# Kernel tuning notes

Hardware: AMD Instinct MI355X
Metric: run time of the kernel (lower is better)

## Reference

```python
import jax, jax.numpy as jnp
import numpy as np

B, F, D = 32, 4096, 256
ALPHA = 0.001


def setup_inputs() -> dict:
    key = jax.random.key(0)
    ks = jax.random.split(key, 9)
    s = 1.0 / np.sqrt(D)
    return {
        "q": jax.random.normal(ks[0], (B, F, D), dtype=jnp.float32),
        "k": jax.random.normal(ks[1], (B, F, D), dtype=jnp.float32),
        "v": jax.random.normal(ks[2], (B, F, D), dtype=jnp.float32),
        "Wq": jax.random.normal(ks[3], (D, D), dtype=jnp.float32) * s,
        "bq": jax.random.normal(ks[4], (D,), dtype=jnp.float32) * 0.01,
        "Wk": jax.random.normal(ks[5], (D, D), dtype=jnp.float32) * s,
        "bk": jax.random.normal(ks[6], (D,), dtype=jnp.float32) * 0.01,
        "Wv": jax.random.normal(ks[7], (D, D), dtype=jnp.float32) * s,
        "bv": jax.random.normal(ks[8], (D,), dtype=jnp.float32) * 0.01,
    }


def reference(q, k, v, Wq, bq, Wk, bk, Wv, bv):
    # nn.Linear: x @ W.T + b
    queries = q @ Wq.T + bq            # [b, f, d]
    keys = k @ Wk.T + bk               # [b, f, d]
    values = v @ Wv.T + bv             # [b, f, d]
    # batched Gram matrix + ridge term
    key_sym = jnp.einsum("bfd,bfe->bde", keys, keys)          # [b, d, d]
    key_sym = key_sym + ALPHA * jnp.eye(D, dtype=key_sym.dtype)
    key_sym_inv = jnp.linalg.inv(key_sym)                      # [b, d, d]
    kkik = jnp.einsum("bde,bfe->bdf", key_sym_inv, keys)       # [b, d, f]
    kkikv = jnp.einsum("bdf,bfe->bde", kkik, values)           # [b, d, d]
    itn = jax.nn.softmax(kkikv, axis=2)                        # sigma=True; softmax over dim 2
    h = jnp.einsum("bfd,bde->be", queries, itn)                # [b, d]
    return h
```

## Files before the change

kernel.cpp:

```cpp
#include <hip/hip_runtime.h>
#include <math.h>

#define FDIM 4096
#define DDIM 256
#define ALPHA_R 0.001f
#define SVH (3 * 32 * 256)

typedef __attribute__((ext_vector_type(8))) short short8;
typedef __attribute__((ext_vector_type(4))) float f32x4;

__device__ __forceinline__ unsigned cvt_pk_bf16(float lo_e, float hi_e) {
  unsigned r;
  asm("v_cvt_pk_bf16_f32 %0, %1, %2" : "=v"(r) : "v"(lo_e), "v"(hi_e));
  return r;
}

__device__ __forceinline__ void hilo8(const float* x, uint4& H, uint4& L) {
  unsigned h0 = cvt_pk_bf16(x[0], x[1]);
  unsigned h1 = cvt_pk_bf16(x[2], x[3]);
  unsigned h2 = cvt_pk_bf16(x[4], x[5]);
  unsigned h3 = cvt_pk_bf16(x[6], x[7]);
  unsigned l0 = cvt_pk_bf16(x[0] - __uint_as_float(h0 << 16),
                            x[1] - __uint_as_float(h0 & 0xFFFF0000u));
  unsigned l1 = cvt_pk_bf16(x[2] - __uint_as_float(h1 << 16),
                            x[3] - __uint_as_float(h1 & 0xFFFF0000u));
  unsigned l2 = cvt_pk_bf16(x[4] - __uint_as_float(h2 << 16),
                            x[5] - __uint_as_float(h2 & 0xFFFF0000u));
  unsigned l3 = cvt_pk_bf16(x[6] - __uint_as_float(h3 << 16),
                            x[7] - __uint_as_float(h3 & 0xFFFF0000u));
  H = make_uint4(h0, h1, h2, h3);
  L = make_uint4(l0, l1, l2, l3);
}

__global__ __launch_bounds__(256) void gram_fused(const float* __restrict__ kg,
                                                  const float* __restrict__ vg,
                                                  const float* __restrict__ qg,
                                                  float* __restrict__ Gp0,
                                                  float* __restrict__ Gp1,
                                                  float* __restrict__ svec,
                                                  float* __restrict__ part) {
  int flat = blockIdx.x;
  int tid = threadIdx.x;

  if (flat >= 1024) {
    int cs = flat - 1024;
    int chunk = cs & 15, b = cs >> 4;
    int rg = tid >> 6, dq = tid & 63;
    const float* p = qg + ((size_t)b * FDIM + chunk * 256 + rg) * DDIM + dq * 4;
    float4 s = make_float4(0.f, 0.f, 0.f, 0.f);
    for (int i = 0; i < 64; ++i) {
      float4 t = *(const float4*)(p + (size_t)i * 4 * DDIM);
      s.x += t.x; s.y += t.y; s.z += t.z; s.w += t.w;
    }
    __shared__ __align__(16) float redq[4][64][4];
    *(float4*)&redq[rg][dq][0] = s;
    __syncthreads();
    if (rg == 0) {
      float4 a0 = *(float4*)&redq[0][dq][0];
      float4 a1 = *(float4*)&redq[1][dq][0];
      float4 a2 = *(float4*)&redq[2][dq][0];
      float4 a3 = *(float4*)&redq[3][dq][0];
      float4 t = make_float4(a0.x + a1.x + a2.x + a3.x, a0.y + a1.y + a2.y + a3.y,
                             a0.z + a1.z + a2.z + a3.z, a0.w + a1.w + a2.w + a3.w);
      *(float4*)(part + ((size_t)chunk * 32 + b) * DDIM + dq * 4) = t;
    }
    return;
  }

  int xcd = flat & 7, s = flat >> 3;
  int b = xcd * 4 + (s >> 5);
  int rem = s & 31;
  int tile = rem >> 1;
  int half = rem & 1;
  int tm = tile >> 2, tn = tile & 3;
  int mBase = tm * 64, nBase = tn * 64;
  const float* Kb = kg + (size_t)b * FDIM * DDIM;
  const float* Vb = vg + (size_t)b * FDIM * DDIM;

  __shared__ __align__(16) unsigned short Ah[64][40], Al[64][40];
  __shared__ __align__(16) unsigned short Bh[64][40], Bl[64][40];
  __shared__ __align__(16) unsigned short Ch[64][40], Cl[64][40];
  __shared__ float sred[4][68];

  int w = tid >> 6, lane = tid & 63;
  int wr = w >> 1, wc = w & 1;
  int lrow = lane & 15;
  int kof = (lane >> 4) * 8;

  const float* pA = Kb + mBase + lane;
  const float* pB = Kb + nBase + lane;
  const float* pC = Vb + nBase + lane;

  bool doK = (tn == 0), doV = (tm == 0);
  float sK = 0.f, sV = 0.f;
  int fBase = half * 2048;

  float xa[8], xb[8], xc[8];
  auto loadIter = [&](int it) {
    int f = fBase + it * 32 + w * 8;
#pragma unroll
    for (int j = 0; j < 8; ++j) {
      xa[j] = pA[(size_t)(f + j) * DDIM];
      xb[j] = pB[(size_t)(f + j) * DDIM];
      xc[j] = pC[(size_t)(f + j) * DDIM];
    }
  };
  auto stash = [&](const float* x, unsigned short (*H)[40], unsigned short (*L)[40]) {
    uint4 hh, ll;
    hilo8(x, hh, ll);
    *(uint4*)&H[lane][w * 8] = hh;
    *(uint4*)&L[lane][w * 8] = ll;
  };

  f32x4 acc0[2][2], acc1[2][2];
#pragma unroll
  for (int mt = 0; mt < 2; ++mt)
#pragma unroll
    for (int nt = 0; nt < 2; ++nt) {
      acc0[mt][nt] = (f32x4){0.f, 0.f, 0.f, 0.f};
      acc1[mt][nt] = (f32x4){0.f, 0.f, 0.f, 0.f};
    }

  loadIter(0);
  for (int it = 0; it < 64; ++it) {
    __syncthreads();
    stash(xa, Ah, Al);
    stash(xb, Bh, Bl);
    stash(xc, Ch, Cl);
    if (doK) sK += ((xa[0] + xa[1]) + (xa[2] + xa[3])) + ((xa[4] + xa[5]) + (xa[6] + xa[7]));
    if (doV) sV += ((xc[0] + xc[1]) + (xc[2] + xc[3])) + ((xc[4] + xc[5]) + (xc[6] + xc[7]));
    __syncthreads();
    if (it < 63) loadIter(it + 1);

    short8 bh[2], bl[2], ch[2], cl[2];
#pragma unroll
    for (int nt = 0; nt < 2; ++nt) {
      int rB = wc * 32 + nt * 16 + lrow;
      bh[nt] = *(const short8*)&Bh[rB][kof];
      bl[nt] = *(const short8*)&Bl[rB][kof];
      ch[nt] = *(const short8*)&Ch[rB][kof];
      cl[nt] = *(const short8*)&Cl[rB][kof];
    }
    __builtin_amdgcn_s_setprio(1);
#pragma unroll
    for (int mt = 0; mt < 2; ++mt) {
      int rA = wr * 32 + mt * 16 + lrow;
      short8 ah = *(const short8*)&Ah[rA][kof];
      short8 al = *(const short8*)&Al[rA][kof];
#pragma unroll
      for (int nt = 0; nt < 2; ++nt) {
        f32x4 t = acc0[mt][nt];
        t = __builtin_amdgcn_mfma_f32_16x16x32_bf16(ah, bh[nt], t, 0, 0, 0);
        t = __builtin_amdgcn_mfma_f32_16x16x32_bf16(ah, bl[nt], t, 0, 0, 0);
        t = __builtin_amdgcn_mfma_f32_16x16x32_bf16(al, bh[nt], t, 0, 0, 0);
        acc0[mt][nt] = t;
        f32x4 u = acc1[mt][nt];
        u = __builtin_amdgcn_mfma_f32_16x16x32_bf16(ah, ch[nt], u, 0, 0, 0);
        u = __builtin_amdgcn_mfma_f32_16x16x32_bf16(ah, cl[nt], u, 0, 0, 0);
        u = __builtin_amdgcn_mfma_f32_16x16x32_bf16(al, ch[nt], u, 0, 0, 0);
        acc1[mt][nt] = u;
      }
    }
    __builtin_amdgcn_s_setprio(0);
  }

  float* Gp = half ? Gp1 : Gp0;
  float* G0 = Gp + ((size_t)b * 2) * 65536;
  float* G1 = G0 + 65536;
#pragma unroll
  for (int mt = 0; mt < 2; ++mt)
#pragma unroll
    for (int nt = 0; nt < 2; ++nt)
#pragma unroll
      for (int r = 0; r < 4; ++r) {
        int row = mBase + wr * 32 + mt * 16 + (lane >> 4) * 4 + r;
        int col = nBase + wc * 32 + nt * 16 + (lane & 15);
        G0[(size_t)row * DDIM + col] = acc0[mt][nt][r];
        G1[(size_t)row * DDIM + col] = acc1[mt][nt][r];
      }

  float* svecH = svec + (size_t)half * SVH;
  if (doK) {
    __syncthreads();
    sred[w][lane] = sK;
    __syncthreads();
    if (tid < 64) {
      float t = sred[0][tid] + sred[1][tid] + sred[2][tid] + sred[3][tid];
      svecH[(size_t)1 * 32 * 256 + (size_t)b * 256 + mBase + tid] = t;
    }
  }
  if (doV) {
    __syncthreads();
    sred[w][lane] = sV;
    __syncthreads();
    if (tid < 64) {
      float t = sred[0][tid] + sred[1][tid] + sred[2][tid] + sred[3][tid];
      svecH[(size_t)2 * 32 * 256 + (size_t)b * 256 + nBase + tid] = t;
    }
  }
}

__global__ void smallvec(const float* __restrict__ Wq, const float* __restrict__ bq,
                         const float* __restrict__ Wk, const float* __restrict__ Wv,
                         const float* __restrict__ part,
                         const float* __restrict__ svec, float* __restrict__ uvec) {
  int b = blockIdx.x; int d = threadIdx.x;
  __shared__ float sq[256], sk[256], sv[256];
  float sqv = 0.f;
  for (int c = 0; c < 16; ++c) sqv += part[((size_t)c * 32 + b) * DDIM + d];
  sq[d] = sqv;
  sk[d] = svec[((size_t)1 * 32 + b) * DDIM + d] + svec[SVH + ((size_t)1 * 32 + b) * DDIM + d];
  sv[d] = svec[((size_t)2 * 32 + b) * DDIM + d] + svec[SVH + ((size_t)2 * 32 + b) * DDIM + d];
  __syncthreads();
  float uk = 0.f, uv = 0.f, uq = 0.f;
  for (int j = 0; j < 256; j += 4) {
    float4 wk4 = *(const float4*)(Wk + (size_t)d * DDIM + j);
    float4 wv4 = *(const float4*)(Wv + (size_t)d * DDIM + j);
    float4 wq4 = *(const float4*)(Wq + (size_t)d * DDIM + j);
    uk += wk4.x * sk[j] + wk4.y * sk[j + 1] + wk4.z * sk[j + 2] + wk4.w * sk[j + 3];
    uv += wv4.x * sv[j] + wv4.y * sv[j + 1] + wv4.z * sv[j + 2] + wv4.w * sv[j + 3];
    uq += wq4.x * sq[j] + wq4.y * sq[j + 1] + wq4.z * sq[j + 2] + wq4.w * sq[j + 3];
  }
  uvec[((size_t)0 * 32 + b) * DDIM + d] = uk;
  uvec[((size_t)1 * 32 + b) * DDIM + d] = uv;
  uvec[((size_t)2 * 32 + b) * DDIM + d] = uq + 4096.f * bq[d];
}

__global__ __launch_bounds__(256) void gemm_pass1(const float* __restrict__ Wk,
                                                  const float* __restrict__ Gp0,
                                                  const float* __restrict__ Gp1,
                                                  float* __restrict__ T) {
  int tile = blockIdx.x, wsel = blockIdx.y, b = blockIdx.z;
  int tm = tile >> 2, tn = tile & 3;
  int mBase = tm * 64, nBase = tn * 64;
  const float* A = Wk;
  const float* B0 = Gp0 + ((size_t)b * 2 + wsel) * 65536;
  const float* B1 = Gp1 + ((size_t)b * 2 + wsel) * 65536;
  float* C = T + ((size_t)b * 2 + wsel) * 65536;

  __shared__ __align__(16) unsigned short Ah[64][40], Al[64][40];
  __shared__ __align__(16) unsigned short Bh[64][40], Bl[64][40];

  int tid = threadIdx.x;
  int w = tid >> 6, lane = tid & 63;
  int wr = w >> 1, wc = w & 1;
  int lrow = lane & 15;
  int kof = (lane >> 4) * 8;
  int ar = tid >> 2, aq = tid & 3;
  const float* pArow = A + (size_t)(mBase + ar) * DDIM + aq * 8;
  int bw = tid >> 6;
  const float* pB0 = B0 + nBase + lane;
  const float* pB1 = B1 + nBase + lane;

  float xa[8], xb[8];
  auto loadIter = [&](int k0) {
    float4 a0 = *(const float4*)(pArow + k0);
    float4 a1 = *(const float4*)(pArow + k0 + 4);
    xa[0] = a0.x; xa[1] = a0.y; xa[2] = a0.z; xa[3] = a0.w;
    xa[4] = a1.x; xa[5] = a1.y; xa[6] = a1.z; xa[7] = a1.w;
#pragma unroll
    for (int j = 0; j < 8; ++j) {
      size_t o = (size_t)(k0 + bw * 8 + j) * DDIM;
      xb[j] = pB0[o] + pB1[o];
    }
  };

  f32x4 acc[2][2];
#pragma unroll
  for (int mt = 0; mt < 2; ++mt)
#pragma unroll
    for (int nt = 0; nt < 2; ++nt) acc[mt][nt] = (f32x4){0.f, 0.f, 0.f, 0.f};

  loadIter(0);
  for (int it = 0; it < 8; ++it) {
    __syncthreads();
    {
      uint4 hh, ll;
      hilo8(xa, hh, ll);
      *(uint4*)&Ah[ar][aq * 8] = hh;
      *(uint4*)&Al[ar][aq * 8] = ll;
      hilo8(xb, hh, ll);
      *(uint4*)&Bh[lane][bw * 8] = hh;
      *(uint4*)&Bl[lane][bw * 8] = ll;
    }
    __syncthreads();
    if (it < 7) loadIter((it + 1) * 32);

    short8 bh[2], bl[2];
#pragma unroll
    for (int nt = 0; nt < 2; ++nt) {
      int rB = wc * 32 + nt * 16 + lrow;
      bh[nt] = *(const short8*)&Bh[rB][kof];
      bl[nt] = *(const short8*)&Bl[rB][kof];
    }
    __builtin_amdgcn_s_setprio(1);
#pragma unroll
    for (int mt = 0; mt < 2; ++mt) {
      int rA = wr * 32 + mt * 16 + lrow;
      short8 ah = *(const short8*)&Ah[rA][kof];
      short8 al = *(const short8*)&Al[rA][kof];
#pragma unroll
      for (int nt = 0; nt < 2; ++nt) {
        f32x4 t = acc[mt][nt];
        t = __builtin_amdgcn_mfma_f32_16x16x32_bf16(ah, bh[nt], t, 0, 0, 0);
        t = __builtin_amdgcn_mfma_f32_16x16x32_bf16(ah, bl[nt], t, 0, 0, 0);
        t = __builtin_amdgcn_mfma_f32_16x16x32_bf16(al, bh[nt], t, 0, 0, 0);
        acc[mt][nt] = t;
      }
    }
    __builtin_amdgcn_s_setprio(0);
  }

#pragma unroll
  for (int mt = 0; mt < 2; ++mt)
#pragma unroll
    for (int nt = 0; nt < 2; ++nt)
#pragma unroll
      for (int r = 0; r < 4; ++r) {
        int row = mBase + wr * 32 + mt * 16 + (lane >> 4) * 4 + r;
        int col = nBase + wc * 32 + nt * 16 + (lane & 15);
        C[(size_t)row * DDIM + col] = acc[mt][nt][r];
      }
}

__global__ __launch_bounds__(256) void gemm_pass2(const float* __restrict__ T,
                                                  const float* __restrict__ Wk,
                                                  const float* __restrict__ Wv,
                                                  float* __restrict__ S,
                                                  const float* __restrict__ uvec,
                                                  const float* __restrict__ bk,
                                                  const float* __restrict__ bv) {
  int tile = blockIdx.x, wsel = blockIdx.y, b = blockIdx.z;
  int tm = tile >> 2, tn = tile & 3;
  int mBase = tm * 64, nBase = tn * 64;
  const float* A = T + ((size_t)b * 2 + wsel) * 65536;
  const float* W = wsel ? Wv : Wk;
  float* C = S + ((size_t)b * 2 + wsel) * 65536;

  __shared__ __align__(16) unsigned short Ah[64][40], Al[64][40];
  __shared__ __align__(16) unsigned short Bh[64][40], Bl[64][40];

  int tid = threadIdx.x;
  int w = tid >> 6, lane = tid & 63;
  int wr = w >> 1, wc = w & 1;
  int lrow = lane & 15;
  int kof = (lane >> 4) * 8;
  int ar = tid >> 2, aq = tid & 3;
  const float* pArow = A + (size_t)(mBase + ar) * DDIM + aq * 8;
  const float* pBrow = W + (size_t)(nBase + ar) * DDIM + aq * 8;

  float xa[8], xb[8];
  auto loadIter = [&](int k0) {
    float4 a0 = *(const float4*)(pArow + k0);
    float4 a1 = *(const float4*)(pArow + k0 + 4);
    xa[0] = a0.x; xa[1] = a0.y; xa[2] = a0.z; xa[3] = a0.w;
    xa[4] = a1.x; xa[5] = a1.y; xa[6] = a1.z; xa[7] = a1.w;
    float4 b0 = *(const float4*)(pBrow + k0);
    float4 b1 = *(const float4*)(pBrow + k0 + 4);
    xb[0] = b0.x; xb[1] = b0.y; xb[2] = b0.z; xb[3] = b0.w;
    xb[4] = b1.x; xb[5] = b1.y; xb[6] = b1.z; xb[7] = b1.w;
  };

  f32x4 acc[2][2];
#pragma unroll
  for (int mt = 0; mt < 2; ++mt)
#pragma unroll
    for (int nt = 0; nt < 2; ++nt) acc[mt][nt] = (f32x4){0.f, 0.f, 0.f, 0.f};

  loadIter(0);
  for (int it = 0; it < 8; ++it) {
    __syncthreads();
    {
      uint4 hh, ll;
      hilo8(xa, hh, ll);
      *(uint4*)&Ah[ar][aq * 8] = hh;
      *(uint4*)&Al[ar][aq * 8] = ll;
      hilo8(xb, hh, ll);
      *(uint4*)&Bh[ar][aq * 8] = hh;
      *(uint4*)&Bl[ar][aq * 8] = ll;
    }
    __syncthreads();
    if (it < 7) loadIter((it + 1) * 32);

    short8 bh[2], bl[2];
#pragma unroll
    for (int nt = 0; nt < 2; ++nt) {
      int rB = wc * 32 + nt * 16 + lrow;
      bh[nt] = *(const short8*)&Bh[rB][kof];
      bl[nt] = *(const short8*)&Bl[rB][kof];
    }
    __builtin_amdgcn_s_setprio(1);
#pragma unroll
    for (int mt = 0; mt < 2; ++mt) {
      int rA = wr * 32 + mt * 16 + lrow;
      short8 ah = *(const short8*)&Ah[rA][kof];
      short8 al = *(const short8*)&Al[rA][kof];
#pragma unroll
      for (int nt = 0; nt < 2; ++nt) {
        f32x4 t = acc[mt][nt];
        t = __builtin_amdgcn_mfma_f32_16x16x32_bf16(ah, bh[nt], t, 0, 0, 0);
        t = __builtin_amdgcn_mfma_f32_16x16x32_bf16(ah, bl[nt], t, 0, 0, 0);
        t = __builtin_amdgcn_mfma_f32_16x16x32_bf16(al, bh[nt], t, 0, 0, 0);
        acc[mt][nt] = t;
      }
    }
    __builtin_amdgcn_s_setprio(0);
  }

  const float* uk = uvec + ((size_t)0 * 32 + b) * DDIM;
  const float* uvv = uvec + ((size_t)1 * 32 + b) * DDIM;
#pragma unroll
  for (int mt = 0; mt < 2; ++mt)
#pragma unroll
    for (int nt = 0; nt < 2; ++nt) {
      int col = nBase + wc * 32 + nt * 16 + (lane & 15);
      float ue = wsel ? uvv[col] : uk[col];
      float be = wsel ? bv[col] : bk[col];
#pragma unroll
      for (int r = 0; r < 4; ++r) {
        int row = mBase + wr * 32 + mt * 16 + (lane >> 4) * 4 + r;
        float add = uk[row] * be + bk[row] * ue + 4096.f * bk[row] * be;
        if (wsel == 0 && row == col) add += ALPHA_R;
        C[(size_t)row * DDIM + col] = acc[mt][nt][r] + add;
      }
    }
}

__global__ __launch_bounds__(1024, 4) void gj_factor(float* __restrict__ Sb,
                                                     float* __restrict__ Mtg) {
  int b = blockIdx.x;
  float* A = Sb + (size_t)b * 2 * 65536;
  int tid = threadIdx.x;
  int r = tid >> 2;
  int q = tid & 3;

  __shared__ __align__(16) float Mt[64][264];
  __shared__ __align__(16) float Sst[64][200];
  __shared__ __align__(16) float prow[2][64];
  __shared__ float fac[2][256];

  for (int pg = 0; pg < 4; ++pg) {
    float x[16];
    {
      const float* Ar = A + (size_t)r * 256 + pg * 64 + q * 16;
#pragma unroll
      for (int m = 0; m < 4; ++m) {
        float4 t = *(const float4*)(Ar + m * 4);
        x[m * 4 + 0] = t.x; x[m * 4 + 1] = t.y;
        x[m * 4 + 2] = t.z; x[m * 4 + 3] = t.w;
      }
    }
    if (r == pg * 64) {
      *(float4*)&prow[0][q * 16 + 0]  = make_float4(x[0], x[1], x[2], x[3]);
      *(float4*)&prow[0][q * 16 + 4]  = make_float4(x[4], x[5], x[6], x[7]);
      *(float4*)&prow[0][q * 16 + 8]  = make_float4(x[8], x[9], x[10], x[11]);
      *(float4*)&prow[0][q * 16 + 12] = make_float4(x[12], x[13], x[14], x[15]);
    }
    if (q == 0) fac[0][r] = x[0];
    __syncthreads();

#pragma unroll
    for (int jo = 0; jo < 4; ++jo) {
#pragma unroll
      for (int ji = 0; ji < 16; ++ji) {
        const int j = jo * 16 + ji;
        const int p = pg * 64 + j;
        const int buf = j & 1, nb = buf ^ 1;
        float piv = fac[buf][p];
        float ip = 1.0f / piv;
        float g = fac[buf][r] * ip;
        bool diag = (r == p);
#pragma unroll
        for (int m = 0; m < 16; ++m) {
          float pv = prow[buf][q * 16 + m];
          x[m] = diag ? pv * ip : fmaf(-g, pv, x[m]);
        }
        if (q == jo) x[ji] = diag ? ip : (0.f - g);
        if (j < 63) {
          const int jn = j + 1;
          if (r == pg * 64 + jn) {
            *(float4*)&prow[nb][q * 16 + 0]  = make_float4(x[0], x[1], x[2], x[3]);
            *(float4*)&prow[nb][q * 16 + 4]  = make_float4(x[4], x[5], x[6], x[7]);
            *(float4*)&prow[nb][q * 16 + 8]  = make_float4(x[8], x[9], x[10], x[11]);
            *(float4*)&prow[nb][q * 16 + 12] = make_float4(x[12], x[13], x[14], x[15]);
          }
          if (q == (jn >> 4)) fac[nb][r] = x[jn & 15];
        }
        __syncthreads();
      }
    }
#pragma unroll
    for (int m = 0; m < 16; ++m) Mt[q * 16 + m][r] = x[m];
    __syncthreads();

    {
      int j = tid >> 4, rseg = (tid & 15) * 16;
      float* dst = Mtg + (((size_t)b * 4 + pg) * 64 + j) * 256 + rseg;
#pragma unroll
      for (int m = 0; m < 4; ++m) {
        float4 t = make_float4(Mt[j][rseg + m * 4 + 0], Mt[j][rseg + m * 4 + 1],
                               Mt[j][rseg + m * 4 + 2], Mt[j][rseg + m * 4 + 3]);
        *(float4*)(dst + m * 4) = t;
      }
    }

    int W = (3 - pg) * 64;
    if (W > 0) {
      int c_off = (pg + 1) * 64;
      {
        int cpt = W >> 4;
        int jr = tid >> 4, tc = tid & 15;
        const float* src = A + (size_t)(pg * 64 + jr) * 256 + c_off + tc * cpt;
        for (int m = 0; m < cpt; m += 4) {
          float4 t = *(const float4*)(src + m);
          *(float4*)&Sst[jr][tc * cpt + m] = t;
        }
      }
      __syncthreads();
      int colTiles = W >> 3;
      int rt = tid / colTiles;
      int ctile = tid - rt * colTiles;
      if (rt < 32) {
        int r0 = rt * 8, c0 = ctile * 8;
        float acc[8][8];
#pragma unroll
        for (int i = 0; i < 8; ++i)
#pragma unroll
          for (int j2 = 0; j2 < 8; ++j2) acc[i][j2] = 0.f;
        for (int j = 0; j < 64; ++j) {
          float4 m0 = *(const float4*)&Mt[j][r0];
          float4 m1 = *(const float4*)&Mt[j][r0 + 4];
          float4 s0 = *(const float4*)&Sst[j][c0];
          float4 s1 = *(const float4*)&Sst[j][c0 + 4];
          float mv[8] = {m0.x, m0.y, m0.z, m0.w, m1.x, m1.y, m1.z, m1.w};
          float sv[8] = {s0.x, s0.y, s0.z, s0.w, s1.x, s1.y, s1.z, s1.w};
#pragma unroll
          for (int i = 0; i < 8; ++i)
#pragma unroll
            for (int j2 = 0; j2 < 8; ++j2)
              acc[i][j2] = fmaf(mv[i], sv[j2], acc[i][j2]);
        }
#pragma unroll
        for (int ii = 0; ii < 8; ++ii) {
          int row = r0 + ii;
          bool inPanel = ((row >> 6) == pg);
          float* dst = A + (size_t)row * 256 + c_off + c0;
          float4 o0 = make_float4(acc[ii][0], acc[ii][1], acc[ii][2], acc[ii][3]);
          float4 o1 = make_float4(acc[ii][4], acc[ii][5], acc[ii][6], acc[ii][7]);
          if (!inPanel) {
            float4 a0 = *(const float4*)(dst);
            float4 a1 = *(const float4*)(dst + 4);
            o0.x += a0.x; o0.y += a0.y; o0.z += a0.z; o0.w += a0.w;
            o1.x += a1.x; o1.y += a1.y; o1.z += a1.z; o1.w += a1.w;
          }
          *(float4*)(dst) = o0;
          *(float4*)(dst + 4) = o1;
        }
      }
      __syncthreads();
    }
  }
}

__global__ __launch_bounds__(256) void gj_apply(float* __restrict__ Sb,
                                                const float* __restrict__ Mtg) {
  int blk = blockIdx.x;
  int b = blk >> 3;
  int cbase = (blk & 7) * 32;
  float* Bm = Sb + ((size_t)b * 2 + 1) * 65536;
  int tid = threadIdx.x;
  int rt = tid >> 3;
  int ct = tid & 7;

  __shared__ __align__(16) float Mt[64][260];
  __shared__ __align__(8) float Bp[64][34];

  float4 breg[8];
#pragma unroll
  for (int i = 0; i < 8; ++i)
    breg[i] = *(const float4*)(Bm + (size_t)(rt * 8 + i) * 256 + cbase + ct * 4);

  for (int pg = 0; pg < 4; ++pg) {
    __syncthreads();
    {
      int j = tid >> 2, seg = (tid & 3) * 64;
      const float* src = Mtg + (((size_t)b * 4 + pg) * 64 + j) * 256 + seg;
#pragma unroll
      for (int m = 0; m < 16; ++m) {
        float4 t = *(const float4*)(src + m * 4);
        *(float4*)&Mt[j][seg + m * 4] = t;
      }
    }
    if (rt >= pg * 8 && rt < (pg + 1) * 8) {
#pragma unroll
      for (int i = 0; i < 8; ++i) {
        int j = (rt - pg * 8) * 8 + i;
        *(float2*)&Bp[j][ct * 4]     = make_float2(breg[i].x, breg[i].y);
        *(float2*)&Bp[j][ct * 4 + 2] = make_float2(breg[i].z, breg[i].w);
      }
    }
    __syncthreads();

    float acc[8][4];
#pragma unroll
    for (int i = 0; i < 8; ++i)
#pragma unroll
      for (int c = 0; c < 4; ++c) acc[i][c] = 0.f;
#pragma unroll 4
    for (int j = 0; j < 64; ++j) {
      float4 m0 = *(const float4*)&Mt[j][rt * 8];
      float4 m1 = *(const float4*)&Mt[j][rt * 8 + 4];
      float2 b0 = *(const float2*)&Bp[j][ct * 4];
      float2 b1 = *(const float2*)&Bp[j][ct * 4 + 2];
      float mv[8] = {m0.x, m0.y, m0.z, m0.w, m1.x, m1.y, m1.z, m1.w};
      float bv4[4] = {b0.x, b0.y, b1.x, b1.y};
#pragma unroll
      for (int i = 0; i < 8; ++i)
#pragma unroll
        for (int c = 0; c < 4; ++c)
          acc[i][c] = fmaf(mv[i], bv4[c], acc[i][c]);
    }
    bool inPanel = ((rt >> 3) == pg);
#pragma unroll
    for (int i = 0; i < 8; ++i) {
      if (inPanel) {
        breg[i] = make_float4(acc[i][0], acc[i][1], acc[i][2], acc[i][3]);
      } else {
        breg[i].x += acc[i][0]; breg[i].y += acc[i][1];
        breg[i].z += acc[i][2]; breg[i].w += acc[i][3];
      }
    }
  }

#pragma unroll
  for (int i = 0; i < 8; ++i)
    *(float4*)(Bm + (size_t)(rt * 8 + i) * 256 + cbase + ct * 4) = breg[i];
}

__global__ void softmax_h(const float* __restrict__ S,
                          const float* __restrict__ uvec,
                          float* __restrict__ out) {
  int b = blockIdx.x;
  const float* X = S + ((size_t)b * 2 + 1) * 65536;
  int tid = threadIdx.x; int lane = tid & 63; int wv = tid >> 6;
  __shared__ float mrow[256], qos[256];
  __shared__ float qs_s[256];
  qs_s[tid] = uvec[((size_t)2 * 32 + b) * DDIM + tid];
  for (int rr = 0; rr < 64; ++rr) {
    int row = rr * 4 + wv;
    float x0 = X[row * 256 + lane];
    float x1 = X[row * 256 + lane + 64];
    float x2 = X[row * 256 + lane + 128];
    float x3 = X[row * 256 + lane + 192];
    float m = fmaxf(fmaxf(x0, x1), fmaxf(x2, x3));
    for (int o = 32; o > 0; o >>= 1) m = fmaxf(m, __shfl_xor(m, o, 64));
    float s = expf(x0 - m) + expf(x1 - m) + expf(x2 - m) + expf(x3 - m);
    for (int o = 32; o > 0; o >>= 1) s += __shfl_xor(s, o, 64);
    if (lane == 0) {
      mrow[row] = m;
      qos[row] = s;
    }
  }
  __syncthreads();
  qos[tid] = qs_s[tid] / qos[tid];
  __syncthreads();
  int e = tid;
  float acc = 0.f;
  for (int d = 0; d < 256; ++d)
    acc += qos[d] * expf(X[d * 256 + e] - mrow[d]);
  out[(size_t)b * 256 + e] = acc;
}

extern "C" void kernel_launch(void* const* d_in, const int* in_sizes, int n_in,
                              void* d_out, int out_size, void* d_ws, size_t ws_size,
                              hipStream_t stream) {
  const float* q  = (const float*)d_in[0];
  const float* k  = (const float*)d_in[1];
  const float* v  = (const float*)d_in[2];
  const float* Wq = (const float*)d_in[3];
  const float* bq = (const float*)d_in[4];
  const float* Wk = (const float*)d_in[5];
  const float* bk = (const float*)d_in[6];
  const float* Wv = (const float*)d_in[7];
  const float* bv = (const float*)d_in[8];
  float* out = (float*)d_out;

  float* ws   = (float*)d_ws;
  float* Gbuf = ws;
  float* Tbuf = Gbuf + (size_t)32 * 2 * 65536;
  float* Sbuf = Tbuf + (size_t)32 * 2 * 65536;
  float* part = Sbuf + (size_t)32 * 2 * 65536;
  float* svec = part + (size_t)16 * 3 * 32 * 256;
  float* uvec = svec + (size_t)2 * 3 * 32 * 256;

  gram_fused<<<1536, 256, 0, stream>>>(k, v, q, Gbuf, Sbuf, svec, part);
  smallvec<<<32, 256, 0, stream>>>(Wq, bq, Wk, Wv, part, svec, uvec);
  gemm_pass1<<<dim3(16, 2, 32), 256, 0, stream>>>(Wk, Gbuf, Sbuf, Tbuf);
  gemm_pass2<<<dim3(16, 2, 32), 256, 0, stream>>>(Tbuf, Wk, Wv, Sbuf, uvec, bk, bv);
  gj_factor<<<32, 1024, 0, stream>>>(Sbuf, Gbuf);
  gj_apply<<<256, 256, 0, stream>>>(Sbuf, Gbuf);
  softmax_h<<<32, 256, 0, stream>>>(Sbuf, uvec, out);
}
```

Measured before the change: 483.6 us.

## Pivot two Gauss-Jordan columns per barrier and add lo*lo bf16 MFMA term

The Gauss-Jordan factor kernel now eliminates two pivot columns per step, computing the second pivot row on the fly from the first. This halves the number of __syncthreads barriers inside the 64-column panel. Separately, both split-bf16 GEMM kernels gain a fourth lo*lo MFMA term, which raises precision but adds a third more matrix instructions in those loops. The fused two-pivot update changes rounding order slightly and adds per-step arithmetic.

Measured after the change: 485.3 us. About the same (+0.4%).

```diff
diff --git a/kernel.cpp b/kernel.cpp
--- a/kernel.cpp
+++ b/kernel.cpp
@@ -305,6 +305,7 @@
         t = __builtin_amdgcn_mfma_f32_16x16x32_bf16(ah, bh[nt], t, 0, 0, 0);
         t = __builtin_amdgcn_mfma_f32_16x16x32_bf16(ah, bl[nt], t, 0, 0, 0);
         t = __builtin_amdgcn_mfma_f32_16x16x32_bf16(al, bh[nt], t, 0, 0, 0);
+        t = __builtin_amdgcn_mfma_f32_16x16x32_bf16(al, bl[nt], t, 0, 0, 0);
         acc[mt][nt] = t;
       }
     }
@@ -401,6 +402,7 @@
         t = __builtin_amdgcn_mfma_f32_16x16x32_bf16(ah, bh[nt], t, 0, 0, 0);
         t = __builtin_amdgcn_mfma_f32_16x16x32_bf16(ah, bl[nt], t, 0, 0, 0);
         t = __builtin_amdgcn_mfma_f32_16x16x32_bf16(al, bh[nt], t, 0, 0, 0);
+        t = __builtin_amdgcn_mfma_f32_16x16x32_bf16(al, bl[nt], t, 0, 0, 0);
         acc[mt][nt] = t;
       }
     }
@@ -436,13 +438,14 @@
 
   __shared__ __align__(16) float Mt[64][264];
   __shared__ __align__(16) float Sst[64][200];
-  __shared__ __align__(16) float prow[2][64];
-  __shared__ float fac[2][256];
+  __shared__ __align__(16) float prow0[2][64], prow1p[2][64];
+  __shared__ float fac0[2][256], fac1p[2][256];
 
   for (int pg = 0; pg < 4; ++pg) {
+    int pg64 = pg * 64;
     float x[16];
     {
-      const float* Ar = A + (size_t)r * 256 + pg * 64 + q * 16;
+      const float* Ar = A + (size_t)r * 256 + pg64 + q * 16;
 #pragma unroll
       for (int m = 0; m < 4; ++m) {
         float4 t = *(const float4*)(Ar + m * 4);
@@ -450,45 +453,71 @@
         x[m * 4 + 2] = t.z; x[m * 4 + 3] = t.w;
       }
     }
-    if (r == pg * 64) {
-      *(float4*)&prow[0][q * 16 + 0]  = make_float4(x[0], x[1], x[2], x[3]);
-      *(float4*)&prow[0][q * 16 + 4]  = make_float4(x[4], x[5], x[6], x[7]);
-      *(float4*)&prow[0][q * 16 + 8]  = make_float4(x[8], x[9], x[10], x[11]);
-      *(float4*)&prow[0][q * 16 + 12] = make_float4(x[12], x[13], x[14], x[15]);
-    }
-    if (q == 0) fac[0][r] = x[0];
-    __syncthreads();
-
-#pragma unroll
-    for (int jo = 0; jo < 4; ++jo) {
-#pragma unroll
-      for (int ji = 0; ji < 16; ++ji) {
-        const int j = jo * 16 + ji;
-        const int p = pg * 64 + j;
-        const int buf = j & 1, nb = buf ^ 1;
-        float piv = fac[buf][p];
-        float ip = 1.0f / piv;
-        float g = fac[buf][r] * ip;
-        bool diag = (r == p);
-#pragma unroll
-        for (int m = 0; m < 16; ++m) {
-          float pv = prow[buf][q * 16 + m];
-          x[m] = diag ? pv * ip : fmaf(-g, pv, x[m]);
+    if (r == pg64) {
+#pragma unroll
+      for (int m4 = 0; m4 < 4; ++m4)
+        *(float4*)&prow0[0][q * 16 + m4 * 4] =
+            make_float4(x[m4 * 4], x[m4 * 4 + 1], x[m4 * 4 + 2], x[m4 * 4 + 3]);
+    }
+    if (r == pg64 + 1) {
+#pragma unroll
+      for (int m4 = 0; m4 < 4; ++m4)
+        *(float4*)&prow1p[0][q * 16 + m4 * 4] =
+            make_float4(x[m4 * 4], x[m4 * 4 + 1], x[m4 * 4 + 2], x[m4 * 4 + 3]);
+    }
+    if (q == 0) { fac0[0][r] = x[0]; fac1p[0][r] = x[1]; }
+    __syncthreads();
+
+#pragma unroll
+    for (int t = 0; t < 32; ++t) {
+      const int buf = t & 1, nb = buf ^ 1;
+      const int j0 = 2 * t, j1 = 2 * t + 1;
+      const int p0g = pg64 + j0, p1g = pg64 + j1;
+      float piv0 = prow0[buf][j0];
+      float ip0 = 1.0f / piv0;
+      float c1 = fac0[buf][p1g] * ip0;
+      float pr0j1 = prow0[buf][j1];
+      float piv1 = fmaf(-c1, pr0j1, prow1p[buf][j1]);
+      float ip1 = 1.0f / piv1;
+      bool d0 = (r == p0g), d1 = (r == p1g);
+      float g0 = fac0[buf][r] * ip0;
+      float f1 = d0 ? ip0 * pr0j1 : fmaf(-g0, pr0j1, fac1p[buf][r]);
+      float g1 = f1 * ip1;
+#pragma unroll
+      for (int m = 0; m < 16; ++m) {
+        float p0v = prow0[buf][q * 16 + m];
+        float p1v = fmaf(-c1, p0v, prow1p[buf][q * 16 + m]);
+        float y = d0 ? p0v * ip0 : fmaf(-g0, p0v, x[m]);
+        float z = d1 ? p1v * ip1 : fmaf(-g1, p1v, y);
+        x[m] = z;
+      }
+      const int jo = j0 >> 4;
+      if (q == jo) {
+        float v0 = d0 ? ip0 : (0.f - g0);
+        float p1_at_j0 = 0.f - c1;
+        x[j0 & 15] = d1 ? p1_at_j0 * ip1 : fmaf(-g1, p1_at_j0, v0);
+        x[j1 & 15] = d1 ? ip1 : (0.f - g1);
+      }
+      if (t < 31) {
+        const int n0 = j0 + 2, n1 = j1 + 2;
+        if (r == pg64 + n0) {
+#pragma unroll
+          for (int m4 = 0; m4 < 4; ++m4)
+            *(float4*)&prow0[nb][q * 16 + m4 * 4] =
+                make_float4(x[m4 * 4], x[m4 * 4 + 1], x[m4 * 4 + 2], x[m4 * 4 + 3]);
         }
-        if (q == jo) x[ji] = diag ? ip : (0.f - g);
-        if (j < 63) {
-          const int jn = j + 1;
-          if (r == pg * 64 + jn) {
-            *(float4*)&prow[nb][q * 16 + 0]  = make_float4(x[0], x[1], x[2], x[3]);
-            *(float4*)&prow[nb][q * 16 + 4]  = make_float4(x[4], x[5], x[6], x[7]);
-            *(float4*)&prow[nb][q * 16 + 8]  = make_float4(x[8], x[9], x[10], x[11]);
-            *(float4*)&prow[nb][q * 16 + 12] = make_float4(x[12], x[13], x[14], x[15]);
-          }
-          if (q == (jn >> 4)) fac[nb][r] = x[jn & 15];
+        if (r == pg64 + n1) {
+#pragma unroll
+          for (int m4 = 0; m4 < 4; ++m4)
+            *(float4*)&prow1p[nb][q * 16 + m4 * 4] =
+                make_float4(x[m4 * 4], x[m4 * 4 + 1], x[m4 * 4 + 2], x[m4 * 4 + 3]);
         }
-        __syncthreads();
-      }
-    }
+        const int jn = n0 >> 4;
+        if (q == jn) { fac0[nb][r] = x[n0 & 15]; fac1p[nb][r] = x[n1 & 15]; }
+      }
+      __syncthreads();
+    }
+
 #pragma unroll
     for (int m = 0; m < 16; ++m) Mt[q * 16 + m][r] = x[m];
     __syncthreads();
@@ -506,11 +535,11 @@
 
     int W = (3 - pg) * 64;
     if (W > 0) {
-      int c_off = (pg + 1) * 64;
+      int c_off = pg64 + 64;
       {
         int cpt = W >> 4;
         int jr = tid >> 4, tc = tid & 15;
-        const float* src = A + (size_t)(pg * 64 + jr) * 256 + c_off + tc * cpt;
+        const float* src = A + (size_t)(pg64 + jr) * 256 + c_off + tc * cpt;
         for (int m = 0; m < cpt; m += 4) {
           float4 t = *(const float4*)(src + m);
           *(float4*)&Sst[jr][tc * cpt + m] = t;
```
